# Kernel optimization log

Measured on AMD Instinct MI355X. Metric: run time of the kernel, lower is better.

Reference implementation:

```python
import jax, jax.numpy as jnp
import numpy as np

B, V, H, L = 2, 256, 128, 3
GROUPS = 32  # GroupNorm32 in the 'normalization' head
EPS = 1e-5


def _layernorm(z, g, b):
    m = jnp.mean(z, -1, keepdims=True)
    v = jnp.var(z, -1, keepdims=True)
    return (z - m) * jax.lax.rsqrt(v + EPS) * g + b


def _forward(x, adj_matrix, emb_type, W_node, b_node, W_eattr, b_eattr, W_ee, b_ee,
             Wu, bu, Wv, bv, Wa, ba, Wb, bb, Wc, bc,
             lnh_g, lnh_b, lne_g, lne_b, plo_g, plo_b, plo_W, plo_bW,
             gn_g, gn_b, W_out, b_out):
    # node embed: Embedding(2,H) lookup -> Linear(H,H)
    h = emb_type[x] @ W_node + b_node                      # B V H
    ea = jnp.transpose(adj_matrix, (0, 2, 3, 1))           # B V V 6
    # edge embed: Linear(6,H) -> Linear(H,H)
    e = (ea @ W_eattr + b_eattr) @ W_ee + b_ee             # B V V H
    # graph = graph[..., -6].long(): binary adjacency channel, no grad
    mask = jax.lax.stop_gradient(ea[..., 0])               # B V V
    for l in range(L):
        h_in, e_in = h, e
        # gated anisotropic GCN layer (DIFUSCO GNNLayer, mode='direct')
        Uh = h @ Wu[l] + bu[l]                             # B V H
        Vh = h @ Wv[l] + bv[l]                             # B V H
        e_new = ((h @ Wa[l] + ba[l])[:, None, :, :]
                 + (h @ Wb[l] + bb[l])[:, :, None, :]
                 + (e @ Wc[l] + bc[l]))                    # B V V H
        gates = jax.nn.sigmoid(e_new) * mask[..., None]    # B V V H
        agg = jnp.einsum('bijh,bjh->bih', gates, Vh)       # gated 'sum' aggregation
        h = jax.nn.relu(_layernorm(Uh + agg, lnh_g[l], lnh_b[l]))
        e = jax.nn.relu(_layernorm(e_new, lne_g[l], lne_b[l]))
        # outer residual (GNNDi.dense_forward) + per_layer_out: LN -> SiLU -> Linear
        h = h_in + h
        e = e_in + (jax.nn.silu(_layernorm(e, plo_g[l], plo_b[l])) @ plo_W[l] + plo_bW[l])
    # head: GroupNorm(32,H) -> ReLU -> Conv2d(H, out_channels, 1) on B H V V
    z = jnp.transpose(e, (0, 3, 1, 2))                     # B H V V
    zg = z.reshape(B, GROUPS, H // GROUPS, V, V)
    mu = jnp.mean(zg, axis=(2, 3, 4), keepdims=True)
    var = jnp.var(zg, axis=(2, 3, 4), keepdims=True)
    z = ((zg - mu) * jax.lax.rsqrt(var + EPS)).reshape(B, H, V, V)
    z = jax.nn.relu(z * gn_g[None, :, None, None] + gn_b[None, :, None, None])
    return jnp.einsum('bchw,oc->bohw', z, W_out) + b_out[None, :, None, None]


def setup_inputs() -> dict:
    key = jax.random.key(0)
    ks = jax.random.split(key, 16)
    nrm = lambda k, s: jax.random.normal(k, s, dtype=jnp.float32) * 0.05
    adj = jnp.concatenate([
        (jax.random.uniform(ks[1], (B, 1, V, V)) < 0.15).astype(jnp.float32),  # channel 0: adjacency
        jax.random.normal(ks[2], (B, 5, V, V), dtype=jnp.float32)], axis=1)
    return {
        'x': jax.random.randint(ks[0], (B, V), 0, 2),
        'adj_matrix': adj,
        'emb_type': nrm(ks[3], (2, H)),
        'W_node': nrm(ks[4], (H, H)), 'b_node': jnp.zeros((H,), jnp.float32),
        'W_eattr': nrm(ks[5], (6, H)), 'b_eattr': jnp.zeros((H,), jnp.float32),
        'W_ee': nrm(ks[6], (H, H)), 'b_ee': jnp.zeros((H,), jnp.float32),
        'Wu': nrm(ks[7], (L, H, H)), 'bu': jnp.zeros((L, H), jnp.float32),
        'Wv': nrm(ks[8], (L, H, H)), 'bv': jnp.zeros((L, H), jnp.float32),
        'Wa': nrm(ks[9], (L, H, H)), 'ba': jnp.zeros((L, H), jnp.float32),
        'Wb': nrm(ks[10], (L, H, H)), 'bb': jnp.zeros((L, H), jnp.float32),
        'Wc': nrm(ks[11], (L, H, H)), 'bc': jnp.zeros((L, H), jnp.float32),
        'lnh_g': jnp.ones((L, H), jnp.float32), 'lnh_b': jnp.zeros((L, H), jnp.float32),
        'lne_g': jnp.ones((L, H), jnp.float32), 'lne_b': jnp.zeros((L, H), jnp.float32),
        'plo_g': jnp.ones((L, H), jnp.float32), 'plo_b': jnp.zeros((L, H), jnp.float32),
        'plo_W': nrm(ks[12], (L, H, H)), 'plo_bW': jnp.zeros((L, H), jnp.float32),
        'gn_g': jnp.ones((H,), jnp.float32), 'gn_b': jnp.zeros((H,), jnp.float32),
        'W_out': nrm(ks[13], (1, H)), 'b_out': jnp.zeros((1,), jnp.float32),
    }


def reference(x, adj_matrix, emb_type, W_node, b_node, W_eattr, b_eattr, W_ee, b_ee,
              Wu, bu, Wv, bv, Wa, ba, Wb, bb, Wc, bc,
              lnh_g, lnh_b, lne_g, lne_b, plo_g, plo_b, plo_W, plo_bW,
              gn_g, gn_b, W_out, b_out):
    return _forward(x, adj_matrix, emb_type, W_node, b_node, W_eattr, b_eattr, W_ee, b_ee,
                    Wu, bu, Wv, bv, Wa, ba, Wb, bb, Wc, bc,
                    lnh_g, lnh_b, lne_g, lne_b, plo_g, plo_b, plo_W, plo_bW,
                    gn_g, gn_b, W_out, b_out)
```

## Files before the change

### kernel.cpp

```cpp
#include <hip/hip_runtime.h>
#include <cstdint>
#include <cstddef>


#define EPSV 1e-5f

typedef __attribute__((ext_vector_type(8))) short short8v;
typedef __attribute__((ext_vector_type(4))) float f32x4;

__device__ __forceinline__ float sigmoidf_(float x) { return 1.f / (1.f + __expf(-x)); }

__device__ __forceinline__ unsigned short f2bf(float x) {
    unsigned int u = __float_as_uint(x);
    unsigned int r = u + 0x7FFFu + ((u >> 16) & 1u);
    return (unsigned short)(r >> 16);
}
__device__ __forceinline__ float bf2f(unsigned short u) {
    return __uint_as_float(((unsigned int)u) << 16);
}
__device__ __forceinline__ unsigned int cvtpk(float a, float b) {
    unsigned int r;
    asm("v_cvt_pk_bf16_f32 %0, %1, %2" : "=v"(r) : "v"(a), "v"(b));
    return r;
}
#define SWZ(row, cb) ((cb) ^ (((row) & 7) << 4))

__global__ void k_prep(const int* __restrict__ x, const float* __restrict__ emb,
                       const float* __restrict__ W_node, const float* __restrict__ b_node,
                       float* __restrict__ h, float* __restrict__ aggB,
                       const float* __restrict__ W_ea, const float* __restrict__ b_ea,
                       const float* __restrict__ W_ee, const float* __restrict__ b_ee,
                       float* __restrict__ Wcb, float* __restrict__ bcb,
                       const float* __restrict__ Wc, const float* __restrict__ PW,
                       unsigned short* __restrict__ WT)
{
    const int blk = blockIdx.x, t = threadIdx.x;
    if (blk < 512) {
        __shared__ float se[128];
        if (t < 128) { se[t] = emb[x[blk]*128 + t]; aggB[blk*128 + t] = 0.f; }
        __syncthreads();
        if (t < 128) {
            float acc = b_node[t];
            for (int k = 0; k < 128; ++k) acc = fmaf(se[k], W_node[k*128+t], acc);
            h[blk*128+t] = acc;
        }
    } else if (blk == 512) {
        if (t < 128) {
            float wc0=0,wc1=0,wc2=0,wc3=0,wc4=0,wc5=0,bv=0;
            for (int m = 0; m < 128; ++m) {
                float we = W_ee[m*128 + t];
                wc0 = fmaf(W_ea[0*128+m], we, wc0);
                wc1 = fmaf(W_ea[1*128+m], we, wc1);
                wc2 = fmaf(W_ea[2*128+m], we, wc2);
                wc3 = fmaf(W_ea[3*128+m], we, wc3);
                wc4 = fmaf(W_ea[4*128+m], we, wc4);
                wc5 = fmaf(W_ea[5*128+m], we, wc5);
                bv  = fmaf(b_ea[m], we, bv);
            }
            Wcb[0*128+t]=wc0; Wcb[1*128+t]=wc1; Wcb[2*128+t]=wc2;
            Wcb[3*128+t]=wc3; Wcb[4*128+t]=wc4; Wcb[5*128+t]=wc5;
            bcb[t] = bv + b_ee[t];
        }
    } else {
        const int m = blk - 513;
        const int l = m >> 1;
        const float* src = (m & 1) ? (PW + (size_t)l*16384) : (Wc + (size_t)l*16384);
        unsigned short* dst = WT + (size_t)m*16384;
        for (int idx = t; idx < 16384; idx += 256) {
            int n = idx >> 7, k = idx & 127;
            dst[idx] = f2bf(src[k*128 + n]);
        }
    }
}

__global__ __launch_bounds__(256) void k_einit(
    const float* __restrict__ adj, const float* __restrict__ Wcb,
    const float* __restrict__ bcb, unsigned short* __restrict__ e)
{
    __shared__ float sAdj[6*256];
    const int blk = blockIdx.x, t = threadIdx.x;
    const int b = blk >> 8, i = blk & 255;
    const float* arow = adj + (size_t)b*393216 + (size_t)i*256;
    for (int idx = t; idx < 1536; idx += 256)
        sAdj[idx] = arow[(idx >> 8)*65536 + (idx & 255)];
    const int ch8 = (t & 15) * 8, jgrp = t >> 4;
    float w[6][8], bb8[8];
    #pragma unroll
    for (int c = 0; c < 8; ++c) bb8[c] = bcb[ch8 + c];
    #pragma unroll
    for (int m = 0; m < 6; ++m)
        #pragma unroll
        for (int c = 0; c < 8; ++c) w[m][c] = Wcb[m*128 + ch8 + c];
    __syncthreads();
    unsigned short* erow = e + (size_t)blk*32768;
    for (int it = 0; it < 16; ++it) {
        const int j = jgrp*16 + it;
        float a[6];
        #pragma unroll
        for (int m = 0; m < 6; ++m) a[m] = sAdj[m*256 + j];
        float v[8];
        #pragma unroll
        for (int c = 0; c < 8; ++c) {
            v[c] = bb8[c];
            #pragma unroll
            for (int m = 0; m < 6; ++m) v[c] = fmaf(a[m], w[m][c], v[c]);
        }
        uint4 o;
        o.x = cvtpk(v[0], v[1]); o.y = cvtpk(v[2], v[3]);
        o.z = cvtpk(v[4], v[5]); o.w = cvtpk(v[6], v[7]);
        *(uint4*)&erow[(size_t)j*128 + ch8] = o;
    }
}

__global__ void k_hgemm(float* __restrict__ h, float* __restrict__ Uh, float* __restrict__ aggB,
    const float* __restrict__ Wu_l, const float* __restrict__ bu_l,
    const float* __restrict__ Wv_l, const float* __restrict__ bv_l,
    const float* __restrict__ Wa_l, const float* __restrict__ ba_l,
    const float* __restrict__ Wb_l, const float* __restrict__ bb_l,
    float* __restrict__ VhT, float* __restrict__ AhT, float* __restrict__ Bh,
    const float* __restrict__ lnh_g, const float* __restrict__ lnh_b, int upd)
{
    __shared__ float sh[128];
    __shared__ float sred[4];
    int blk = blockIdx.x, t = threadIdx.x;
    int b = blk >> 8, v = blk & 255;
    float hv_ = h[blk*128 + t];
    if (upd) {
        float val = Uh[blk*128 + t] + aggB[blk*128 + t];
        aggB[blk*128 + t] = 0.f;
        float s = val, q = val*val;
        #pragma unroll
        for (int off = 32; off; off >>= 1) { s += __shfl_down(s, off); q += __shfl_down(q, off); }
        if ((t & 63) == 0) { sred[t>>6] = s; sred[2 + (t>>6)] = q; }
        __syncthreads();
        s = sred[0] + sred[1]; q = sred[2] + sred[3];
        float mean = s * (1.f/128.f);
        float var  = q * (1.f/128.f) - mean*mean;
        float nv = (val - mean) * rsqrtf(var + EPSV) * lnh_g[t] + lnh_b[t];
        hv_ += fmaxf(nv, 0.f);
        h[blk*128 + t] = hv_;
    }
    sh[t] = hv_;
    __syncthreads();
    float au=bu_l[t], av=bv_l[t], aa=ba_l[t], ab=bb_l[t];
    for (int k = 0; k < 128; ++k) {
        float hv = sh[k];
        au = fmaf(hv, Wu_l[k*128+t], au);
        av = fmaf(hv, Wv_l[k*128+t], av);
        aa = fmaf(hv, Wa_l[k*128+t], aa);
        ab = fmaf(hv, Wb_l[k*128+t], ab);
    }
    Uh[blk*128+t]=au; Bh[blk*128+t]=ab;
    VhT[(size_t)(b*128+t)*256 + v] = av;
    AhT[(size_t)(b*128+t)*256 + v] = aa;
}

template<int DO_AGG>
__global__ __launch_bounds__(256) void k_layer(
    unsigned short* __restrict__ e,
    const unsigned short* __restrict__ WcT, const unsigned short* __restrict__ PWT,
    const float* __restrict__ bc_l,
    const float* __restrict__ AhT, const float* __restrict__ Bh,
    const float* __restrict__ VhT, const float* __restrict__ adj,
    const float* __restrict__ lne_g, const float* __restrict__ lne_b,
    const float* __restrict__ plo_g, const float* __restrict__ plo_b,
    const float* __restrict__ pbW_l,
    float* __restrict__ aggB)
{
    __shared__ __align__(16) char sW[32768];
    __shared__ float sRedA[512];

    const int t = threadIdx.x;
    const int bi = blockIdx.x >> 2, chunk = blockIdx.x & 3;
    const int b = bi >> 8, i = bi & 255;
    const int w = t >> 6, lane = t & 63;
    const int lane16 = lane & 15, g = lane >> 4;
    const size_t rowbase = (size_t)bi * 32768;
    const int j0 = chunk*64 + w*16;
    char* sE = sW + w*4096;

    short8v a8[4];
    {
        const unsigned short* arow = e + rowbase + (size_t)(j0 + lane16)*128 + g*8;
        #pragma unroll
        for (int kst = 0; kst < 4; ++kst)
            a8[kst] = *(const short8v*)&arow[kst*32];
    }

    #pragma unroll
    for (int p = 0; p < 8; ++p) {
        const int idx = t*8 + p*2048;
        const int n = idx >> 7, cb = (idx & 127) << 1;
        *(short8v*)(sW + n*256 + SWZ(n, cb)) = *(const short8v*)&WcT[idx];
    }
    __syncthreads();

    f32x4 tv[8];
    float agg[8];
    float s1[4] = {0,0,0,0}, q1[4] = {0,0,0,0};
    const int jb = j0 + g*4;
    float4 mk;
    if (DO_AGG) mk = *(const float4*)&adj[(size_t)b*393216 + (size_t)i*256 + jb];
    const float* mkp = (const float*)&mk;
    #pragma unroll
    for (int nt = 0; nt < 8; ++nt) {
        const int col = nt*16 + lane16;
        f32x4 acc = {0.f,0.f,0.f,0.f};
        #pragma unroll
        for (int kst = 0; kst < 4; ++kst) {
            short8v bfr = *(const short8v*)(sW + col*256 + SWZ(col, kst*64 + g*16));
            acc = __builtin_amdgcn_mfma_f32_16x16x32_bf16(a8[kst], bfr, acc, 0, 0, 0);
        }
        const float bcB = bc_l[col] + Bh[bi*128 + col];
        const float4 ah = *(const float4*)&AhT[(size_t)(b*128+col)*256 + jb];
        const float* ahp = (const float*)&ah;
        if (DO_AGG) {
            const float4 vh = *(const float4*)&VhT[(size_t)(b*128+col)*256 + jb];
            const float* vhp = (const float*)&vh;
            float a = 0.f;
            #pragma unroll
            for (int r = 0; r < 4; ++r) {
                float tvl = acc[r] + bcB + ahp[r];
                a = fmaf(mkp[r]*sigmoidf_(tvl), vhp[r], a);
                s1[r] += tvl; q1[r] = fmaf(tvl, tvl, q1[r]);
                tv[nt][r] = tvl;
            }
            agg[nt] = a;
        } else {
            #pragma unroll
            for (int r = 0; r < 4; ++r) {
                float tvl = acc[r] + bcB + ahp[r];
                s1[r] += tvl; q1[r] = fmaf(tvl, tvl, q1[r]);
                tv[nt][r] = tvl;
            }
        }
    }
    float mu1[4], rs1[4];
    #pragma unroll
    for (int r = 0; r < 4; ++r) {
        float s = s1[r], q = q1[r];
        s += __shfl_xor(s,1); q += __shfl_xor(q,1);
        s += __shfl_xor(s,2); q += __shfl_xor(q,2);
        s += __shfl_xor(s,4); q += __shfl_xor(q,4);
        s += __shfl_xor(s,8); q += __shfl_xor(q,8);
        float mu = s*(1.f/128.f);
        mu1[r] = mu; rs1[r] = rsqrtf(q*(1.f/128.f) - mu*mu + EPSV);
    }
    float s2[4] = {0,0,0,0}, q2[4] = {0,0,0,0};
    #pragma unroll
    for (int nt = 0; nt < 8; ++nt) {
        const int col = nt*16 + lane16;
        const float lg = lne_g[col], lb = lne_b[col];
        #pragma unroll
        for (int r = 0; r < 4; ++r) {
            float tp = fmaxf(fmaf((tv[nt][r]-mu1[r])*rs1[r], lg, lb), 0.f);
            tv[nt][r] = tp;
            s2[r] += tp; q2[r] = fmaf(tp, tp, q2[r]);
        }
    }
    float mu2[4], rs2[4];
    #pragma unroll
    for (int r = 0; r < 4; ++r) {
        float s = s2[r], q = q2[r];
        s += __shfl_xor(s,1); q += __shfl_xor(q,1);
        s += __shfl_xor(s,2); q += __shfl_xor(q,2);
        s += __shfl_xor(s,4); q += __shfl_xor(q,4);
        s += __shfl_xor(s,8); q += __shfl_xor(q,8);
        float mu = s*(1.f/128.f);
        mu2[r] = mu; rs2[r] = rsqrtf(q*(1.f/128.f) - mu*mu + EPSV);
    }

    __syncthreads();

    #pragma unroll
    for (int nt = 0; nt < 8; ++nt) {
        const int col = nt*16 + lane16;
        const float pg = plo_g[col], pb = plo_b[col];
        float u[4];
        #pragma unroll
        for (int r = 0; r < 4; ++r) {
            float uu = fmaf((tv[nt][r]-mu2[r])*rs2[r], pg, pb);
            u[r] = uu * sigmoidf_(uu);
        }
        const unsigned int p01 = cvtpk(u[0], u[1]);
        const unsigned int p23 = cvtpk(u[2], u[3]);
        const int r0 = g*4;
        *(unsigned short*)(sE + (r0+0)*256 + SWZ(r0+0, col*2)) = (unsigned short)p01;
        *(unsigned short*)(sE + (r0+1)*256 + SWZ(r0+1, col*2)) = (unsigned short)(p01 >> 16);
        *(unsigned short*)(sE + (r0+2)*256 + SWZ(r0+2, col*2)) = (unsigned short)p23;
        *(unsigned short*)(sE + (r0+3)*256 + SWZ(r0+3, col*2)) = (unsigned short)(p23 >> 16);
    }
    short8v b8[4];
    #pragma unroll
    for (int kst = 0; kst < 4; ++kst)
        b8[kst] = *(const short8v*)(sE + lane16*256 + SWZ(lane16, kst*64 + g*16));

    __syncthreads();
    #pragma unroll
    for (int p = 0; p < 8; ++p) {
        const int idx = t*8 + p*2048;
        const int n = idx >> 7, cb = (idx & 127) << 1;
        *(short8v*)(sW + n*256 + SWZ(n, cb)) = *(const short8v*)&PWT[idx];
    }
    __syncthreads();

    const int jg = j0 + lane16;
    #pragma unroll
    for (int nt = 0; nt < 8; ++nt) {
        const int an = nt*16 + lane16;
        f32x4 acc = {0.f,0.f,0.f,0.f};
        #pragma unroll
        for (int kst = 0; kst < 4; ++kst) {
            short8v aw = *(const short8v*)(sW + an*256 + SWZ(an, kst*64 + g*16));
            acc = __builtin_amdgcn_mfma_f32_16x16x32_bf16(aw, b8[kst], acc, 0, 0, 0);
        }
        const int n0 = nt*16 + g*4;
        const float4 pw4 = *(const float4*)&pbW_l[n0];
        const float* pwp = (const float*)&pw4;
        unsigned short* ep = &e[rowbase + (size_t)jg*128 + n0];
        const ushort4 ev = *(const ushort4*)ep;
        const float o0 = acc[0] + (pwp[0] + bf2f(ev.x));
        const float o1 = acc[1] + (pwp[1] + bf2f(ev.y));
        const float o2 = acc[2] + (pwp[2] + bf2f(ev.z));
        const float o3 = acc[3] + (pwp[3] + bf2f(ev.w));
        uint2 st;
        st.x = cvtpk(o0, o1);
        st.y = cvtpk(o2, o3);
        *(uint2*)ep = st;
    }

    if (DO_AGG) {
        #pragma unroll
        for (int nt = 0; nt < 8; ++nt) {
            float a = agg[nt];
            a += __shfl_xor(a, 16); a += __shfl_xor(a, 32);
            if (lane < 16) sRedA[w*128 + nt*16 + lane] = a;
        }
        __syncthreads();
        if (t < 128) {
            float S = sRedA[t] + sRedA[128+t] + sRedA[256+t] + sRedA[384+t];
            atomicAdd(&aggB[bi*128 + t], S);
        }
    }
}

__global__ __launch_bounds__(256) void k_gstats(
    const unsigned short* __restrict__ e, float* __restrict__ gsum, float* __restrict__ gsq)
{
    __shared__ float sS[2048], sQ[2048];
    const int blk = blockIdx.x, t = threadIdx.x;
    const int b = blk >> 8;
    const unsigned short* erow = e + (size_t)blk*32768;
    const int ch8 = (t & 15)*8, jgrp = t >> 4;
    float s[8], q[8];
    #pragma unroll
    for (int c = 0; c < 8; ++c) { s[c] = 0.f; q[c] = 0.f; }
    for (int it = 0; it < 16; ++it) {
        const int j = jgrp*16 + it;
        short8v v = *(const short8v*)&erow[(size_t)j*128 + ch8];
        #pragma unroll
        for (int c = 0; c < 8; ++c) {
            float f = bf2f((unsigned short)v[c]);
            s[c] += f; q[c] = fmaf(f, f, q[c]);
        }
    }
    #pragma unroll
    for (int c = 0; c < 8; ++c) { sS[jgrp*128 + ch8 + c] = s[c]; sQ[jgrp*128 + ch8 + c] = q[c]; }
    __syncthreads();
    if (t < 128) {
        float S = 0.f, Q = 0.f;
        #pragma unroll
        for (int r = 0; r < 16; ++r) { S += sS[r*128 + t]; Q += sQ[r*128 + t]; }
        atomicAdd(&gsum[b*128 + t], S);
        atomicAdd(&gsq[b*128 + t], Q);
    }
}

__global__ void k_gfin(const float* __restrict__ gsum, const float* __restrict__ gsq,
                       float* __restrict__ gmu, float* __restrict__ grs)
{
    int t = threadIdx.x;
    int b = t >> 5, g = t & 31;
    int base = b*128 + g*4;
    float s = gsum[base]+gsum[base+1]+gsum[base+2]+gsum[base+3];
    float q = gsq[base]+gsq[base+1]+gsq[base+2]+gsq[base+3];
    const float invN = 1.f/(4.f*65536.f);
    float mu = s*invN;
    float var = q*invN - mu*mu;
    gmu[t] = mu;
    grs[t] = rsqrtf(var + EPSV);
}

__global__ __launch_bounds__(256) void k_head(
    const unsigned short* __restrict__ e, const float* __restrict__ gmu,
    const float* __restrict__ grs, const float* __restrict__ gn_g,
    const float* __restrict__ gn_b, const float* __restrict__ W_out,
    const float* __restrict__ b_out, float* __restrict__ out)
{
    const int blk = blockIdx.x, t = threadIdx.x;
    const int b = blk >> 8;
    const int ch8 = (t & 15)*8, jgrp = t >> 4;
    float gg[8], gb[8], wo[8];
    #pragma unroll
    for (int c = 0; c < 8; ++c) {
        const int ch = ch8 + c;
        const float mu = gmu[b*32 + (ch>>2)], rs = grs[b*32 + (ch>>2)];
        gg[c] = gn_g[ch]*rs;
        gb[c] = gn_b[ch] - mu*gg[c];
        wo[c] = W_out[ch];
    }
    const float bo = b_out[0];
    const unsigned short* erow = e + (size_t)blk*32768;
    float* orow = out + (size_t)blk*256;
    for (int it = 0; it < 16; ++it) {
        const int j = jgrp*16 + it;
        short8v v = *(const short8v*)&erow[(size_t)j*128 + ch8];
        float p = 0.f;
        #pragma unroll
        for (int c = 0; c < 8; ++c) {
            float f = bf2f((unsigned short)v[c]);
            p = fmaf(fmaxf(fmaf(f, gg[c], gb[c]), 0.f), wo[c], p);
        }
        p += __shfl_xor(p, 1); p += __shfl_xor(p, 2);
        p += __shfl_xor(p, 4); p += __shfl_xor(p, 8);
        if ((t & 15) == 0) orow[j] = p + bo;
    }
}

extern "C" void kernel_launch(void* const* d_in, const int* in_sizes, int n_in,
                              void* d_out, int out_size, void* d_ws, size_t ws_size,
                              hipStream_t stream)
{
    const int*   x      = (const int*)  d_in[0];
    const float* adj    = (const float*)d_in[1];
    const float* emb    = (const float*)d_in[2];
    const float* W_node = (const float*)d_in[3];
    const float* b_node = (const float*)d_in[4];
    const float* W_ea   = (const float*)d_in[5];
    const float* b_ea   = (const float*)d_in[6];
    const float* W_ee   = (const float*)d_in[7];
    const float* b_ee   = (const float*)d_in[8];
    const float* Wu     = (const float*)d_in[9];
    const float* bu     = (const float*)d_in[10];
    const float* Wv     = (const float*)d_in[11];
    const float* bv     = (const float*)d_in[12];
    const float* Wa     = (const float*)d_in[13];
    const float* ba     = (const float*)d_in[14];
    const float* Wb     = (const float*)d_in[15];
    const float* bb     = (const float*)d_in[16];
    const float* Wc     = (const float*)d_in[17];
    const float* bc     = (const float*)d_in[18];
    const float* lnh_g  = (const float*)d_in[19];
    const float* lnh_b  = (const float*)d_in[20];
    const float* lne_g  = (const float*)d_in[21];
    const float* lne_b  = (const float*)d_in[22];
    const float* plo_g  = (const float*)d_in[23];
    const float* plo_b  = (const float*)d_in[24];
    const float* plo_W  = (const float*)d_in[25];
    const float* plo_bW = (const float*)d_in[26];
    const float* gn_g   = (const float*)d_in[27];
    const float* gn_b   = (const float*)d_in[28];
    const float* W_out  = (const float*)d_in[29];
    const float* b_out  = (const float*)d_in[30];
    float* out = (float*)d_out;

    float* ws = (float*)d_ws;
    size_t off = 0;
    unsigned short* e = (unsigned short*)(ws + off); off += 8388608;
    float* h    = ws + off; off += 65536;
    float* Uh   = ws + off; off += 65536;
    float* Bh   = ws + off; off += 65536;
    float* VhT  = ws + off; off += 65536;
    float* AhT  = ws + off; off += 65536;
    float* aggB = ws + off; off += 65536;
    float* Wcb  = ws + off; off += 768;
    float* bcb  = ws + off; off += 128;
    float* gsum = ws + off; off += 256;
    float* gsq  = ws + off; off += 256;
    float* gmu  = ws + off; off += 64;
    float* grs  = ws + off; off += 64;
    unsigned short* WT = (unsigned short*)(ws + off); off += 49152;

    k_prep<<<519, 256, 0, stream>>>(x, emb, W_node, b_node, h, aggB,
                                    W_ea, b_ea, W_ee, b_ee, Wcb, bcb,
                                    Wc, plo_W, WT);
    k_einit<<<512, 256, 0, stream>>>(adj, Wcb, bcb, e);
    hipMemsetAsync(gsum, 0, 512*sizeof(float), stream);

    for (int l = 0; l < 3; ++l) {
        k_hgemm<<<512, 128, 0, stream>>>(h, Uh, aggB,
            Wu + (size_t)l*16384, bu + l*128,
            Wv + (size_t)l*16384, bv + l*128,
            Wa + (size_t)l*16384, ba + l*128,
            Wb + (size_t)l*16384, bb + l*128,
            VhT, AhT, Bh,
            lnh_g + (l==0?0:(l-1)*128), lnh_b + (l==0?0:(l-1)*128), l > 0 ? 1 : 0);
        if (l < 2) {
            k_layer<1><<<2048, 256, 0, stream>>>(e,
                WT + (size_t)(2*l)*16384, WT + (size_t)(2*l+1)*16384,
                bc + l*128, AhT, Bh, VhT, adj,
                lne_g + l*128, lne_b + l*128,
                plo_g + l*128, plo_b + l*128,
                plo_bW + l*128, aggB);
        } else {
            k_layer<0><<<2048, 256, 0, stream>>>(e,
                WT + (size_t)(2*l)*16384, WT + (size_t)(2*l+1)*16384,
                bc + l*128, AhT, Bh, VhT, adj,
                lne_g + l*128, lne_b + l*128,
                plo_g + l*128, plo_b + l*128,
                plo_bW + l*128, aggB);
        }
    }

    k_gstats<<<512, 256, 0, stream>>>(e, gsum, gsq);
    k_gfin<<<1, 64, 0, stream>>>(gsum, gsq, gmu, grs);
    k_head<<<512, 256, 0, stream>>>(e, gmu, grs, gn_g, gn_b, W_out, b_out, out);
}
```

Before: 233.4 us.

## Fuse edge init into first layer and GroupNorm stats into last layer

Removes the separate edge-embedding init kernel: the first layer kernel now recomputes the initial edge features from the six adjacency channels and the precomputed combined weights, both for the MFMA A-operand and for the residual. The last layer kernel also accumulates per-group sum and sum of squares through shuffles and shared memory, with atomics into a small per-(batch, group) buffer, so the standalone stats kernel goes away. This saves a full write and reread of the bf16 edge tensor at init and one full read at the end. In exchange, the first layer does redundant small FMAs and strided adjacency loads. Stats now come from fp32 outputs before bf16 rounding, which changes numerics slightly.

```diff
diff --git a/kernel.cpp b/kernel.cpp
--- a/kernel.cpp
+++ b/kernel.cpp
@@ -73,45 +73,6 @@
     }
 }
 
-__global__ __launch_bounds__(256) void k_einit(
-    const float* __restrict__ adj, const float* __restrict__ Wcb,
-    const float* __restrict__ bcb, unsigned short* __restrict__ e)
-{
-    __shared__ float sAdj[6*256];
-    const int blk = blockIdx.x, t = threadIdx.x;
-    const int b = blk >> 8, i = blk & 255;
-    const float* arow = adj + (size_t)b*393216 + (size_t)i*256;
-    for (int idx = t; idx < 1536; idx += 256)
-        sAdj[idx] = arow[(idx >> 8)*65536 + (idx & 255)];
-    const int ch8 = (t & 15) * 8, jgrp = t >> 4;
-    float w[6][8], bb8[8];
-    #pragma unroll
-    for (int c = 0; c < 8; ++c) bb8[c] = bcb[ch8 + c];
-    #pragma unroll
-    for (int m = 0; m < 6; ++m)
-        #pragma unroll
-        for (int c = 0; c < 8; ++c) w[m][c] = Wcb[m*128 + ch8 + c];
-    __syncthreads();
-    unsigned short* erow = e + (size_t)blk*32768;
-    for (int it = 0; it < 16; ++it) {
-        const int j = jgrp*16 + it;
-        float a[6];
-        #pragma unroll
-        for (int m = 0; m < 6; ++m) a[m] = sAdj[m*256 + j];
-        float v[8];
-        #pragma unroll
-        for (int c = 0; c < 8; ++c) {
-            v[c] = bb8[c];
-            #pragma unroll
-            for (int m = 0; m < 6; ++m) v[c] = fmaf(a[m], w[m][c], v[c]);
-        }
-        uint4 o;
-        o.x = cvtpk(v[0], v[1]); o.y = cvtpk(v[2], v[3]);
-        o.z = cvtpk(v[4], v[5]); o.w = cvtpk(v[6], v[7]);
-        *(uint4*)&erow[(size_t)j*128 + ch8] = o;
-    }
-}
-
 __global__ void k_hgemm(float* __restrict__ h, float* __restrict__ Uh, float* __restrict__ aggB,
     const float* __restrict__ Wu_l, const float* __restrict__ bu_l,
     const float* __restrict__ Wv_l, const float* __restrict__ bv_l,
@@ -155,7 +116,7 @@
     AhT[(size_t)(b*128+t)*256 + v] = aa;
 }
 
-template<int DO_AGG>
+template<int EINIT, int DO_AGG, int DO_STATS>
 __global__ __launch_bounds__(256) void k_layer(
     unsigned short* __restrict__ e,
     const unsigned short* __restrict__ WcT, const unsigned short* __restrict__ PWT,
@@ -165,10 +126,13 @@
     const float* __restrict__ lne_g, const float* __restrict__ lne_b,
     const float* __restrict__ plo_g, const float* __restrict__ plo_b,
     const float* __restrict__ pbW_l,
-    float* __restrict__ aggB)
+    float* __restrict__ aggB,
+    const float* __restrict__ Wcb, const float* __restrict__ bcb,
+    float* __restrict__ ggsum, float* __restrict__ ggsq)
 {
     __shared__ __align__(16) char sW[32768];
     __shared__ float sRedA[512];
+    __shared__ float sRedB[512];
 
     const int t = threadIdx.x;
     const int bi = blockIdx.x >> 2, chunk = blockIdx.x & 3;
@@ -180,7 +144,30 @@
     char* sE = sW + w*4096;
 
     short8v a8[4];
-    {
+    float am[6];
+    if (EINIT) {
+        const float* adjp = adj + (size_t)b*393216 + (size_t)i*256 + (j0 + lane16);
+        #pragma unroll
+        for (int m = 0; m < 6; ++m) am[m] = adjp[(size_t)m*65536];
+        #pragma unroll
+        for (int kst = 0; kst < 4; ++kst) {
+            short8v v;
+            #pragma unroll
+            for (int e2 = 0; e2 < 4; ++e2) {
+                const int h0 = kst*32 + g*8 + e2*2;
+                float v0 = bcb[h0], v1 = bcb[h0+1];
+                #pragma unroll
+                for (int m = 0; m < 6; ++m) {
+                    v0 = fmaf(am[m], Wcb[m*128 + h0],     v0);
+                    v1 = fmaf(am[m], Wcb[m*128 + h0 + 1], v1);
+                }
+                const unsigned int p = cvtpk(v0, v1);
+                v[e2*2]   = (short)(unsigned short)p;
+                v[e2*2+1] = (short)(unsigned short)(p >> 16);
+            }
+            a8[kst] = v;
+        }
+    } else {
         const unsigned short* arow = e + rowbase + (size_t)(j0 + lane16)*128 + g*8;
         #pragma unroll
         for (int kst = 0; kst < 4; ++kst)
@@ -305,6 +292,7 @@
     __syncthreads();
 
     const int jg = j0 + lane16;
+    float gs[8], gq[8];
     #pragma unroll
     for (int nt = 0; nt < 8; ++nt) {
         const int an = nt*16 + lane16;
@@ -318,11 +306,27 @@
         const float4 pw4 = *(const float4*)&pbW_l[n0];
         const float* pwp = (const float*)&pw4;
         unsigned short* ep = &e[rowbase + (size_t)jg*128 + n0];
-        const ushort4 ev = *(const ushort4*)ep;
-        const float o0 = acc[0] + (pwp[0] + bf2f(ev.x));
-        const float o1 = acc[1] + (pwp[1] + bf2f(ev.y));
-        const float o2 = acc[2] + (pwp[2] + bf2f(ev.z));
-        const float o3 = acc[3] + (pwp[3] + bf2f(ev.w));
+        float res[4];
+        if (EINIT) {
+            #pragma unroll
+            for (int r = 0; r < 4; ++r) {
+                float v0 = bcb[n0 + r];
+                #pragma unroll
+                for (int m = 0; m < 6; ++m) v0 = fmaf(am[m], Wcb[m*128 + n0 + r], v0);
+                res[r] = v0;
+            }
+        } else {
+            const ushort4 ev = *(const ushort4*)ep;
+            res[0] = bf2f(ev.x); res[1] = bf2f(ev.y); res[2] = bf2f(ev.z); res[3] = bf2f(ev.w);
+        }
+        const float o0 = acc[0] + (pwp[0] + res[0]);
+        const float o1 = acc[1] + (pwp[1] + res[1]);
+        const float o2 = acc[2] + (pwp[2] + res[2]);
+        const float o3 = acc[3] + (pwp[3] + res[3]);
+        if (DO_STATS) {
+            gs[nt] = (o0 + o1) + (o2 + o3);
+            gq[nt] = fmaf(o0,o0, fmaf(o1,o1, fmaf(o2,o2, o3*o3)));
+        }
         uint2 st;
         st.x = cvtpk(o0, o1);
         st.y = cvtpk(o2, o3);
@@ -342,48 +346,34 @@
             atomicAdd(&aggB[bi*128 + t], S);
         }
     }
-}
-
-__global__ __launch_bounds__(256) void k_gstats(
-    const unsigned short* __restrict__ e, float* __restrict__ gsum, float* __restrict__ gsq)
-{
-    __shared__ float sS[2048], sQ[2048];
-    const int blk = blockIdx.x, t = threadIdx.x;
-    const int b = blk >> 8;
-    const unsigned short* erow = e + (size_t)blk*32768;
-    const int ch8 = (t & 15)*8, jgrp = t >> 4;
-    float s[8], q[8];
-    #pragma unroll
-    for (int c = 0; c < 8; ++c) { s[c] = 0.f; q[c] = 0.f; }
-    for (int it = 0; it < 16; ++it) {
-        const int j = jgrp*16 + it;
-        short8v v = *(const short8v*)&erow[(size_t)j*128 + ch8];
-        #pragma unroll
-        for (int c = 0; c < 8; ++c) {
-            float f = bf2f((unsigned short)v[c]);
-            s[c] += f; q[c] = fmaf(f, f, q[c]);
-        }
-    }
-    #pragma unroll
-    for (int c = 0; c < 8; ++c) { sS[jgrp*128 + ch8 + c] = s[c]; sQ[jgrp*128 + ch8 + c] = q[c]; }
-    __syncthreads();
-    if (t < 128) {
-        float S = 0.f, Q = 0.f;
-        #pragma unroll
-        for (int r = 0; r < 16; ++r) { S += sS[r*128 + t]; Q += sQ[r*128 + t]; }
-        atomicAdd(&gsum[b*128 + t], S);
-        atomicAdd(&gsq[b*128 + t], Q);
-    }
-}
-
-__global__ void k_gfin(const float* __restrict__ gsum, const float* __restrict__ gsq,
+    if (DO_STATS) {
+        #pragma unroll
+        for (int nt = 0; nt < 8; ++nt) {
+            float a = gs[nt], qq = gq[nt];
+            a += __shfl_xor(a, 1); qq += __shfl_xor(qq, 1);
+            a += __shfl_xor(a, 2); qq += __shfl_xor(qq, 2);
+            a += __shfl_xor(a, 4); qq += __shfl_xor(qq, 4);
+            a += __shfl_xor(a, 8); qq += __shfl_xor(qq, 8);
+            if (lane16 == 0) {
+                sRedA[w*32 + nt*4 + g] = a;
+                sRedB[w*32 + nt*4 + g] = qq;
+            }
+        }
+        __syncthreads();
+        if (t < 32) {
+            float S = sRedA[t] + sRedA[32+t] + sRedA[64+t] + sRedA[96+t];
+            float Q = sRedB[t] + sRedB[32+t] + sRedB[64+t] + sRedB[96+t];
+            atomicAdd(&ggsum[b*32 + t], S);
+            atomicAdd(&ggsq[b*32 + t], Q);
+        }
+    }
+}
+
+__global__ void k_gfin(const float* __restrict__ ggsum, const float* __restrict__ ggsq,
                        float* __restrict__ gmu, float* __restrict__ grs)
 {
     int t = threadIdx.x;
-    int b = t >> 5, g = t & 31;
-    int base = b*128 + g*4;
-    float s = gsum[base]+gsum[base+1]+gsum[base+2]+gsum[base+3];
-    float q = gsq[base]+gsq[base+1]+gsq[base+2]+gsq[base+3];
+    float s = ggsum[t], q = ggsq[t];
     const float invN = 1.f/(4.f*65536.f);
     float mu = s*invN;
     float var = q*invN - mu*mu;
@@ -475,8 +465,8 @@
     float* aggB = ws + off; off += 65536;
     float* Wcb  = ws + off; off += 768;
     float* bcb  = ws + off; off += 128;
-    float* gsum = ws + off; off += 256;
-    float* gsq  = ws + off; off += 256;
+    float* ggsum = ws + off; off += 64;
+    float* ggsq  = ws + off; off += 64;
     float* gmu  = ws + off; off += 64;
     float* grs  = ws + off; off += 64;
     unsigned short* WT = (unsigned short*)(ws + off); off += 49152;
@@ -484,8 +474,7 @@
     k_prep<<<519, 256, 0, stream>>>(x, emb, W_node, b_node, h, aggB,
                                     W_ea, b_ea, W_ee, b_ee, Wcb, bcb,
                                     Wc, plo_W, WT);
-    k_einit<<<512, 256, 0, stream>>>(adj, Wcb, bcb, e);
-    hipMemsetAsync(gsum, 0, 512*sizeof(float), stream);
+    hipMemsetAsync(ggsum, 0, 512, stream);
 
     for (int l = 0; l < 3; ++l) {
         k_hgemm<<<512, 128, 0, stream>>>(h, Uh, aggB,
@@ -495,24 +484,29 @@
             Wb + (size_t)l*16384, bb + l*128,
             VhT, AhT, Bh,
             lnh_g + (l==0?0:(l-1)*128), lnh_b + (l==0?0:(l-1)*128), l > 0 ? 1 : 0);
-        if (l < 2) {
-            k_layer<1><<<2048, 256, 0, stream>>>(e,
-                WT + (size_t)(2*l)*16384, WT + (size_t)(2*l+1)*16384,
+        const unsigned short* WcT_l = WT + (size_t)(2*l)*16384;
+        const unsigned short* PWT_l = WT + (size_t)(2*l+1)*16384;
+        if (l == 0) {
+            k_layer<1,1,0><<<2048, 256, 0, stream>>>(e, WcT_l, PWT_l,
                 bc + l*128, AhT, Bh, VhT, adj,
                 lne_g + l*128, lne_b + l*128,
                 plo_g + l*128, plo_b + l*128,
-                plo_bW + l*128, aggB);
-        } else {
-            k_layer<0><<<2048, 256, 0, stream>>>(e,
-                WT + (size_t)(2*l)*16384, WT + (size_t)(2*l+1)*16384,
+                plo_bW + l*128, aggB, Wcb, bcb, ggsum, ggsq);
+        } else if (l == 1) {
+            k_layer<0,1,0><<<2048, 256, 0, stream>>>(e, WcT_l, PWT_l,
                 bc + l*128, AhT, Bh, VhT, adj,
                 lne_g + l*128, lne_b + l*128,
                 plo_g + l*128, plo_b + l*128,
-                plo_bW + l*128, aggB);
-        }
-    }
-
-    k_gstats<<<512, 256, 0, stream>>>(e, gsum, gsq);
-    k_gfin<<<1, 64, 0, stream>>>(gsum, gsq, gmu, grs);
+                plo_bW + l*128, aggB, Wcb, bcb, ggsum, ggsq);
+        } else {
+            k_layer<0,0,1><<<2048, 256, 0, stream>>>(e, WcT_l, PWT_l,
+                bc + l*128, AhT, Bh, VhT, adj,
+                lne_g + l*128, lne_b + l*128,
+                plo_g + l*128, plo_b + l*128,
+                plo_bW + l*128, aggB, Wcb, bcb, ggsum, ggsq);
+        }
+    }
+
+    k_gfin<<<1, 64, 0, stream>>>(ggsum, ggsq, gmu, grs);
     k_head<<<512, 256, 0, stream>>>(e, gmu, grs, gn_g, gn_b, W_out, b_out, out);
 }
```

Result: no change. 234.5 us (+0.5%).
